# Kernel tuning notes

Measured on AMD Instinct MI355X. Metric: run time of the kernel, lower is better.

Reference implementation:

```python
import jax, jax.numpy as jnp
import numpy as np

B, NX, NQ, NU = 32768, 512, 128, 64
STD = 0.02


def setup_inputs() -> dict:
    key = jax.random.key(0)
    ks = jax.random.split(key, 8)
    p = lambda k, sh: jax.random.normal(k, sh, dtype=jnp.float32) * STD
    xi = jax.random.normal(ks[0], (B, NX), dtype=jnp.float32)
    u = jax.random.normal(ks[1], (B, NU), dtype=jnp.float32)
    A = p(ks[2], (NX, NX))
    B1 = p(ks[3], (NX, NQ))
    B2 = p(ks[4], (NX, NU))
    C1 = p(ks[5], (NQ, NX))
    # D11 from updateParameters is strictly lower triangular (inv(Lambda) @ tril(H4,-1)),
    # which is what makes the forward substitution loop well-posed.
    D11 = jnp.tril(p(ks[6], (NQ, NQ)), -1)
    D12 = p(ks[7], (NQ, NU))
    # bias=False in __init__ -> zero biases (non-trainable in torch, harmless here)
    bx = jnp.zeros((NX,), dtype=jnp.float32)
    bv = jnp.zeros((NQ,), dtype=jnp.float32)
    return dict(xi=xi, u=u, A=A, B1=B1, B2=B2, C1=C1, D11=D11, D12=D12, bx=bx, bv=bv)


def reference(xi, u, A, B1, B2, C1, D11, D12, bx, bv):
    # Hoist the parts of v_i that do not depend on w out of the recurrence:
    # v_i = xi @ C1[i] + u @ D12[i] + bv[i] + w @ D11[i]
    base = xi @ C1.T + u @ D12.T + bv          # [B, nq]
    nq = D11.shape[0]
    w0 = jnp.zeros_like(base)                   # [B, nq]

    # Sequential forward substitution over the nq nonlinear states.
    # Unset entries of w are zero, exactly matching the torch loop (D11 is
    # strictly lower triangular so only already-computed entries contribute).
    def step(w, xs):
        i, d_row, b_col = xs                    # d_row: [nq], b_col: [B]
        v = b_col + w @ d_row                   # [B]
        return w.at[:, i].set(jnp.tanh(v)), None

    w, _ = jax.lax.scan(step, w0, (jnp.arange(nq), D11, base.T))

    # xi_{+} = A xi + B1 w + B2 u + bx
    return xi @ A.T + w @ B1.T + u @ B2.T + bx
```

## Files before the change

kernel.cpp:

```cpp
#include <hip/hip_runtime.h>
#include <hip/hip_bf16.h>

#define BSZ 32768
#define NXD 512
#define NQD 128
#define NUD 64

typedef __attribute__((ext_vector_type(8))) unsigned short u16x8;
typedef __attribute__((ext_vector_type(8))) __bf16 bf16x8;
typedef __attribute__((ext_vector_type(4))) float f32x4;

#define DEVINL static __device__ __forceinline__

DEVINL unsigned short f2bf(float x) {
  __bf16 h = (__bf16)x;
  return __builtin_bit_cast(unsigned short, h);
}

DEVINL void gload_lds16(const ushort* g, ushort* l) {
  __builtin_amdgcn_global_load_lds(
      (const __attribute__((address_space(1))) void*)g,
      (__attribute__((address_space(3))) void*)l, 16, 0, 0);
}

DEVINL bf16x8 ld_frag(const ushort* p) {
  return __builtin_bit_cast(bf16x8, *(const u16x8*)p);
}

DEVINL float tanh_fast(float x) {
  x = fminf(fmaxf(x, -15.f), 15.f);
  float e = __expf(2.f * x);
  return 1.f - 2.f / (e + 1.f);
}

DEVINL void cvt8(const float* src, ushort* dst, int i) {
  const float4* s = (const float4*)src;
  float4 a = s[i * 2], b = s[i * 2 + 1];
  u16x8 v;
  v[0] = f2bf(a.x); v[1] = f2bf(a.y); v[2] = f2bf(a.z); v[3] = f2bf(a.w);
  v[4] = f2bf(b.x); v[5] = f2bf(b.y); v[6] = f2bf(b.z); v[7] = f2bf(b.w);
  *(u16x8*)(dst + (size_t)i * 8) = v;
}

__global__ __launch_bounds__(256) void prep(
    const float* __restrict__ xi, const float* __restrict__ u,
    const float* __restrict__ A, const float* __restrict__ B1,
    const float* __restrict__ B2, const float* __restrict__ C1,
    const float* __restrict__ D11, const float* __restrict__ D12,
    ushort* __restrict__ xib, ushort* __restrict__ ub,
    ushort* __restrict__ Wv, ushort* __restrict__ Wo,
    float* __restrict__ Dt) {
  int idx = blockIdx.x * 256 + threadIdx.x;
  const int N0 = BSZ * NXD / 8;
  const int N1 = N0 + BSZ * NUD / 8;
  const int N2 = N1 + NQD * (NXD + NUD);
  const int N3 = N2 + NXD * 704;
  const int N4 = N3 + NQD * NQD;
  if (idx < N0) {
    cvt8(xi, xib, idx);
  } else if (idx < N1) {
    cvt8(u, ub, idx - N0);
  } else if (idx < N2) {
    int f = idx - N1;
    int i = f / (NXD + NUD);
    int k = f - i * (NXD + NUD);
    Wv[f] = f2bf(k < NXD ? C1[i * NXD + k] : D12[i * NUD + (k - NXD)]);
  } else if (idx < N3) {
    int f = idx - N2;
    int n = f / 704;
    int k = f - n * 704;
    float v;
    if (k < NXD)            v = A[n * NXD + k];
    else if (k < NXD + NQD) v = B1[n * NQD + (k - NXD)];
    else                    v = B2[n * NUD + (k - NXD - NQD)];
    Wo[f] = f2bf(v);
  } else if (idx < N4) {
    int f = idx - N3;
    int j = f >> 7, i = f & (NQD - 1);
    Dt[f] = D11[i * NQD + j];
  }
}

template <int BM, int BN, int WM, int WN>
__global__ __launch_bounds__(WM* WN * 64, 2) void gemm2ph(
    const ushort* __restrict__ p0, int e0, int ld0,
    const ushort* __restrict__ p1, int e1, int ld1,
    const ushort* __restrict__ p2, int ld2,
    const ushort* __restrict__ W, int K,
    const float* __restrict__ biasN,
    float* __restrict__ out, int ldo) {
  constexpr int THREADS = WM * WN * 64;
  constexpr int BK = 64;
  constexpr int MREP = BM / WM / 16;
  constexpr int NREP = BN / WN / 16;
  constexpr int PASSA = BM * 8 / THREADS;
  constexpr int PASSB = BN * 8 / THREADS;

  __shared__ ushort ldsA[2][BM * BK];
  __shared__ ushort ldsB[2][BN * BK];

  const int tid = threadIdx.x;
  const int lane = tid & 63;
  const int wv = tid >> 6;
  const int wm = wv / WN, wn = wv % WN;
  const int rowBase = blockIdx.x * BM;
  const int colBase = blockIdx.y * BN;

  f32x4 acc[MREP][NREP];
#pragma unroll
  for (int m = 0; m < MREP; ++m)
#pragma unroll
    for (int n = 0; n < NREP; ++n) acc[m][n] = (f32x4){0.f, 0.f, 0.f, 0.f};

  const int NT = K / BK;

  auto stage = [&](int b, int kt) {
    const int k0 = kt * BK;
    const ushort* src; int kk, ld;
    if (k0 < e0)      { src = p0; kk = k0;      ld = ld0; }
    else if (k0 < e1) { src = p1; kk = k0 - e0; ld = ld1; }
    else              { src = p2; kk = k0 - e1; ld = ld2; }
#pragma unroll
    for (int p = 0; p < PASSA; ++p) {
      int idx = p * THREADS + tid;
      int row = idx >> 3, slot = idx & 7;
      int gcol = kk + ((slot ^ (row & 7)) << 3);
      gload_lds16(src + (size_t)(rowBase + row) * ld + gcol,
                  &ldsA[b][idx * 8]);
    }
#pragma unroll
    for (int p = 0; p < PASSB; ++p) {
      int idx = p * THREADS + tid;
      int row = idx >> 3, slot = idx & 7;
      int gcol = k0 + ((slot ^ (row & 7)) << 3);
      gload_lds16(W + (size_t)(colBase + row) * K + gcol, &ldsB[b][idx * 8]);
    }
  };

  stage(0, 0);
  __syncthreads();

  int cur = 0;
  for (int kt = 0; kt < NT; ++kt) {
    if (kt + 1 < NT) stage(cur ^ 1, kt + 1);

#pragma unroll
    for (int ks = 0; ks < 2; ++ks) {
      bf16x8 af[MREP], bfr[NREP];
#pragma unroll
      for (int m = 0; m < MREP; ++m) {
        int r = wm * (BM / WM) + m * 16 + (lane & 15);
        int slot = (ks * 4 + (lane >> 4)) ^ (r & 7);
        af[m] = ld_frag(&ldsA[cur][r * BK + slot * 8]);
      }
#pragma unroll
      for (int n = 0; n < NREP; ++n) {
        int r = wn * (BN / WN) + n * 16 + (lane & 15);
        int slot = (ks * 4 + (lane >> 4)) ^ (r & 7);
        bfr[n] = ld_frag(&ldsB[cur][r * BK + slot * 8]);
      }
#pragma unroll
      for (int m = 0; m < MREP; ++m)
#pragma unroll
        for (int n = 0; n < NREP; ++n)
          acc[m][n] = __builtin_amdgcn_mfma_f32_16x16x32_bf16(
              af[m], bfr[n], acc[m][n], 0, 0, 0);
    }
    __syncthreads();
    cur ^= 1;
  }

  const int cl = lane & 15;
  const int rq = (lane >> 4) * 4;
#pragma unroll
  for (int m = 0; m < MREP; ++m) {
    int row = rowBase + wm * (BM / WM) + m * 16 + rq;
#pragma unroll
    for (int n = 0; n < NREP; ++n) {
      int col = colBase + wn * (BN / WN) + n * 16 + cl;
      float bn = biasN[col];
      float* o = out + (size_t)row * ldo + col;
#pragma unroll
      for (int j = 0; j < 4; ++j) o[(size_t)j * ldo] = acc[m][n][j] + bn;
    }
  }
}

__global__ __launch_bounds__(512) void recur16(const float* __restrict__ base,
                                               const float* __restrict__ Dt,
                                               ushort* __restrict__ wout) {
  __shared__ float ldsD[NQD * NQD];
  const int tid = threadIdx.x;

  for (int c = tid; c < NQD * NQD / 4; c += 512) {
    int j = c >> 5, ch = c & 31;
    int slot = ((ch & 1) << 4) | (ch >> 1);
    ((float4*)ldsD)[j * 32 + slot] = ((const float4*)Dt)[c];
  }
  __syncthreads();

  const int lane = tid & 63;
  const int wid = tid >> 6;
  const int s = lane & 15;
  const int g = lane >> 4;
  const int row = blockIdx.x * 32 + wid * 4 + g;

  float acc[8];
  {
    const float4* bp4 = (const float4*)(base + (size_t)row * NQD + s * 8);
    float4 a0 = bp4[0], a1 = bp4[1];
    acc[0] = a0.x; acc[1] = a0.y; acc[2] = a0.z; acc[3] = a0.w;
    acc[4] = a1.x; acc[5] = a1.y; acc[6] = a1.z; acc[7] = a1.w;
  }
  float wl[8];
#pragma unroll
  for (int t = 0; t < 8; ++t) wl[t] = 0.f;

  const float4* ldsD4 = (const float4*)ldsD;

  for (int jb = 0; jb < 16; ++jb) {
    const int ownerLane = (g << 4) | jb;
    const bool own = (s == jb);
#pragma unroll
    for (int jj = 0; jj < 8; ++jj) {
      float tv = tanh_fast(acc[jj]);
      float wj = __shfl(tv, ownerLane, 64);
      if (own) wl[jj] = wj;
      const int jrow = (jb * 8 + jj) * 32;
      float4 d0 = ldsD4[jrow + s];
      float4 d1 = ldsD4[jrow + 16 + s];
      acc[0] += d0.x * wj; acc[1] += d0.y * wj;
      acc[2] += d0.z * wj; acc[3] += d0.w * wj;
      acc[4] += d1.x * wj; acc[5] += d1.y * wj;
      acc[6] += d1.z * wj; acc[7] += d1.w * wj;
    }
  }

  ushort* orow = wout + (size_t)row * NQD + s * 8;
  u16x8 v;
#pragma unroll
  for (int t = 0; t < 8; ++t) v[t] = f2bf(wl[t]);
  *(u16x8*)orow = v;
}

extern "C" void kernel_launch(void* const* d_in, const int* in_sizes, int n_in,
                              void* d_out, int out_size, void* d_ws, size_t ws_size,
                              hipStream_t stream) {
  const float* xi  = (const float*)d_in[0];
  const float* u   = (const float*)d_in[1];
  const float* A   = (const float*)d_in[2];
  const float* B1  = (const float*)d_in[3];
  const float* B2  = (const float*)d_in[4];
  const float* C1  = (const float*)d_in[5];
  const float* D11 = (const float*)d_in[6];
  const float* D12 = (const float*)d_in[7];
  const float* bx  = (const float*)d_in[8];
  const float* bv  = (const float*)d_in[9];
  float* out = (float*)d_out;

  char* ws = (char*)d_ws;
  ushort* xib  = (ushort*)(ws + 0);
  ushort* ub   = (ushort*)(ws + 33554432);
  ushort* wb   = (ushort*)(ws + 37748736);
  float*  base = (float*)(ws + 46137344);
  ushort* Wv   = (ushort*)(ws + 62914560);
  ushort* Wo   = (ushort*)(ws + 63062016);
  float*  Dt   = (float*)(ws + 63782912);

  {
    int total = BSZ * NXD / 8 + BSZ * NUD / 8 + NQD * (NXD + NUD) + NXD * 704 +
                NQD * NQD;
    prep<<<dim3((total + 255) / 256), 256, 0, stream>>>(
        xi, u, A, B1, B2, C1, D11, D12, xib, ub, Wv, Wo, Dt);
  }

  gemm2ph<128, 128, 2, 2><<<dim3(BSZ / 128, 1), 256, 0, stream>>>(
      xib, NXD, NXD, ub, NXD + NUD, NUD, ub, NUD, Wv, NXD + NUD, bv, base, NQD);

  recur16<<<dim3(BSZ / 32), 512, 0, stream>>>(base, Dt, wb);

  gemm2ph<256, 256, 2, 4><<<dim3(BSZ / 256, NXD / 256), 512, 0, stream>>>(
      xib, NXD, NXD, wb, NXD + NQD, NQD, ub, NUD, Wo, NXD + NQD + NUD, bx, out,
      NXD);
}
```

Measured before the change: 229.3 us.

## Restructure recurrence kernel to 8 lanes per row with triangular skip

The forward-substitution kernel now assigns 8 lanes per batch row instead of 16, so each block covers 64 rows and half as many blocks launch. The loop over the 128 states is fully unrolled and skips D11 columns that can no longer be affected, exploiting the lower-triangular structure. Computed w values are stored in place in the accumulator registers, which removes the separate wl array and the swizzled LDS layout. tanh now uses hardware exp2 and reciprocal without input clamping, trading some accuracy and a larger register and code footprint for fewer instructions.

```diff
diff --git a/kernel.cpp b/kernel.cpp
--- a/kernel.cpp
+++ b/kernel.cpp
@@ -28,9 +28,9 @@
 }
 
 DEVINL float tanh_fast(float x) {
-  x = fminf(fmaxf(x, -15.f), 15.f);
-  float e = __expf(2.f * x);
-  return 1.f - 2.f / (e + 1.f);
+  float e2 = __builtin_amdgcn_exp2f(x * 2.88539008f);
+  float r = __builtin_amdgcn_rcpf(e2 + 1.f);
+  return __builtin_fmaf(-2.f, r, 1.f);
 }
 
 DEVINL void cvt8(const float* src, ushort* dst, int i) {
@@ -186,61 +186,57 @@
   }
 }
 
-__global__ __launch_bounds__(512) void recur16(const float* __restrict__ base,
-                                               const float* __restrict__ Dt,
-                                               ushort* __restrict__ wout) {
+__global__ __launch_bounds__(512) void recur8(const float* __restrict__ base,
+                                              const float* __restrict__ Dt,
+                                              ushort* __restrict__ wout) {
   __shared__ float ldsD[NQD * NQD];
   const int tid = threadIdx.x;
-
-  for (int c = tid; c < NQD * NQD / 4; c += 512) {
-    int j = c >> 5, ch = c & 31;
-    int slot = ((ch & 1) << 4) | (ch >> 1);
-    ((float4*)ldsD)[j * 32 + slot] = ((const float4*)Dt)[c];
-  }
+  for (int c = tid; c < NQD * NQD / 4; c += 512)
+    ((float4*)ldsD)[c] = ((const float4*)Dt)[c];
   __syncthreads();
 
   const int lane = tid & 63;
   const int wid = tid >> 6;
-  const int s = lane & 15;
-  const int g = lane >> 4;
-  const int row = blockIdx.x * 32 + wid * 4 + g;
-
-  float acc[8];
+  const int s = lane & 7;
+  const int grp = lane >> 3;
+  const int row = blockIdx.x * 64 + wid * 8 + grp;
+  const int laneBase = lane & 56;
+
+  float4 acc[4];
   {
-    const float4* bp4 = (const float4*)(base + (size_t)row * NQD + s * 8);
-    float4 a0 = bp4[0], a1 = bp4[1];
-    acc[0] = a0.x; acc[1] = a0.y; acc[2] = a0.z; acc[3] = a0.w;
-    acc[4] = a1.x; acc[5] = a1.y; acc[6] = a1.z; acc[7] = a1.w;
-  }
-  float wl[8];
-#pragma unroll
-  for (int t = 0; t < 8; ++t) wl[t] = 0.f;
-
-  const float4* ldsD4 = (const float4*)ldsD;
-
-  for (int jb = 0; jb < 16; ++jb) {
-    const int ownerLane = (g << 4) | jb;
-    const bool own = (s == jb);
-#pragma unroll
-    for (int jj = 0; jj < 8; ++jj) {
-      float tv = tanh_fast(acc[jj]);
-      float wj = __shfl(tv, ownerLane, 64);
-      if (own) wl[jj] = wj;
-      const int jrow = (jb * 8 + jj) * 32;
-      float4 d0 = ldsD4[jrow + s];
-      float4 d1 = ldsD4[jrow + 16 + s];
-      acc[0] += d0.x * wj; acc[1] += d0.y * wj;
-      acc[2] += d0.z * wj; acc[3] += d0.w * wj;
-      acc[4] += d1.x * wj; acc[5] += d1.y * wj;
-      acc[6] += d1.z * wj; acc[7] += d1.w * wj;
-    }
-  }
-
-  ushort* orow = wout + (size_t)row * NQD + s * 8;
-  u16x8 v;
-#pragma unroll
-  for (int t = 0; t < 8; ++t) v[t] = f2bf(wl[t]);
-  *(u16x8*)orow = v;
+    const float4* bp4 = (const float4*)(base + (size_t)row * NQD);
+#pragma unroll
+    for (int k = 0; k < 4; ++k) acc[k] = bp4[s + 8 * k];
+  }
+
+  const float4* D4 = (const float4*)ldsD;
+
+#pragma unroll
+  for (int j = 0; j < NQD; ++j) {
+    const int src = (j >> 2) & 7;
+    const int r = j >> 5;
+    const int e = j & 3;
+    float tv = tanh_fast(acc[r][e]);
+    float wj = __shfl(tv, laneBase | src, 64);
+    if (s == src) acc[r][e] = wj;
+#pragma unroll
+    for (int k = 0; k < 4; ++k) {
+      if (j < 32 * k + 32) {
+        float4 d = D4[j * 32 + s + 8 * k];
+        acc[k].x += d.x * wj; acc[k].y += d.y * wj;
+        acc[k].z += d.z * wj; acc[k].w += d.w * wj;
+      }
+    }
+  }
+
+  ushort* orow = wout + (size_t)row * NQD;
+#pragma unroll
+  for (int k = 0; k < 4; ++k) {
+    ushort4 v;
+    v.x = f2bf(acc[k].x); v.y = f2bf(acc[k].y);
+    v.z = f2bf(acc[k].z); v.w = f2bf(acc[k].w);
+    *(ushort4*)(orow + 4 * (s + 8 * k)) = v;
+  }
 }
 
 extern "C" void kernel_launch(void* const* d_in, const int* in_sizes, int n_in,
@@ -277,7 +273,7 @@
   gemm2ph<128, 128, 2, 2><<<dim3(BSZ / 128, 1), 256, 0, stream>>>(
       xib, NXD, NXD, ub, NXD + NUD, NUD, ub, NUD, Wv, NXD + NUD, bv, base, NQD);
 
-  recur16<<<dim3(BSZ / 32), 512, 0, stream>>>(base, Dt, wb);
+  recur8<<<dim3(BSZ / 64), 512, 0, stream>>>(base, Dt, wb);
 
   gemm2ph<256, 256, 2, 4><<<dim3(BSZ / 256, NXD / 256), 512, 0, stream>>>(
       xib, NXD, NXD, wb, NXD + NQD, NQD, ub, NUD, Wo, NXD + NQD + NUD, bx, out,
```

Result: faster. 211.9 us (-7.6%).
